# Kernel optimization log

Measured on AMD Instinct MI355X. Metric: run time of the kernel, lower is better.

The kernel has to match this reference:

```python
import jax, jax.numpy as jnp
import numpy as np


def _xcorr3x3_valid(x, k):
    # x: [B,H,W], k: [B,3,3] per-sample kernel; cross-correlation (matches F.conv2d), VALID padding
    B, H, W = x.shape
    out = jnp.zeros((B, H - 2, W - 2), dtype=x.dtype)
    for u in range(3):
        for v in range(3):
            out = out + x[:, u:u + H - 2, v:v + W - 2] * k[:, u, v, None, None]
    return out


def setup_inputs() -> dict:
    key = jax.random.key(0)
    ks = jax.random.split(key, 4)
    B, H, W = 256, 256, 256
    pred = jax.random.normal(ks[0], (B, H, W), dtype=jnp.float32)
    rhs = jax.random.normal(ks[1], (B, H - 2, W - 2), dtype=jnp.float32)
    Laplace_kernel = jax.random.normal(ks[2], (B, 3, 3), dtype=jnp.float32)
    Df_dr_kernel = jax.random.normal(ks[3], (B, 3, 3), dtype=jnp.float32)
    # physically sensible meshgrids: R in [1,2] (avoids div-by-zero), Z in [-1,1]
    r = jnp.linspace(1.0, 2.0, W, dtype=jnp.float32)
    z = jnp.linspace(-1.0, 1.0, H, dtype=jnp.float32)
    RR = jnp.broadcast_to(r[None, None, :], (B, H, W)).astype(jnp.float32)
    ZZ = jnp.broadcast_to(z[None, :, None], (B, H, W)).astype(jnp.float32)
    Gauss_kernel = (jnp.array([[1., 2., 1.], [2., 4., 2.], [1., 2., 1.]], dtype=jnp.float32) / 16.0)
    return {"pred": pred, "rhs": rhs, "Laplace_kernel": Laplace_kernel,
            "Df_dr_kernel": Df_dr_kernel, "RR": RR, "ZZ": ZZ, "Gauss_kernel": Gauss_kernel}


def reference(pred, rhs, Laplace_kernel, Df_dr_kernel, RR, ZZ, Gauss_kernel):
    # Lpsi, Dpsi_dr: per-sample 3x3 VALID stencils -> [B, H-2, W-2]
    Lpsi = _xcorr3x3_valid(pred, Laplace_kernel)
    Dpsi_dr = -_xcorr3x3_valid(pred, Df_dr_kernel)
    Dpsi_dr = Dpsi_dr / RR[:, 1:-1, 1:-1]
    lhs = Lpsi - Dpsi_dr
    hr = (RR[:, 1, 2] - RR[:, 1, 1])[:, None, None]
    hz = (ZZ[:, 2, 1] - ZZ[:, 1, 1])[:, None, None]
    alfa = -2.0 * (hr ** 2 + hz ** 2)
    GS_ope = lhs * alfa / (hr ** 2 * hz ** 2)
    # Gaussian smoothing, shared kernel, SAME padding (cross-correlation; kernel is symmetric)
    sm = jax.lax.conv_general_dilated(
        GS_ope[:, None, :, :], Gauss_kernel[None, None, :, :],
        window_strides=(1, 1), padding='SAME')
    GS_ope_smooth = -sm
    rhs_computed = -GS_ope_smooth[:, 0, :, :]
    return jnp.mean((rhs_computed - rhs) ** 2)
```

## Files before the change

kernel.cpp:

```cpp
#include <hip/hip_runtime.h>


__device__ __forceinline__ void g2lds16(const float* g, float* l) {
    __builtin_amdgcn_global_load_lds(
        (const __attribute__((address_space(1))) void*)g,
        (__attribute__((address_space(3))) void*)l,
        16 , 0, 0);
}

__global__ __launch_bounds__(256)
void pde_loss_kernel(const float* __restrict__ pred,
                     const float* __restrict__ rhs,
                     const float* __restrict__ KL,
                     const float* __restrict__ KD,
                     const float* __restrict__ RR,
                     const float* __restrict__ ZZ,
                     float* __restrict__ partials)
{
    constexpr int H = 256, W = 256, OH = 254, OW = 254;
    __shared__ float lds[36 * 256 + 16];
    __shared__ float wsum[4];

    const int tid = threadIdx.x;
    const int l   = tid & 63;
    const int wv  = tid >> 6;
    const int b   = blockIdx.x >> 3;
    const int rb  = (blockIdx.x & 7) * 32;
    const int o0  = rb + wv * 8;
    const int o1  = (o0 + 8 < OH) ? (o0 + 8) : OH;
    const int c0  = 4 * l;

    const size_t ib = (size_t)b * H * W;
    const float* predb = pred + ib;
    const float* rhsb  = rhs + (size_t)b * OH * OW;

    float2 r0[8], r1[8];
#pragma unroll
    for (int j = 0; j < 8; ++j) {
        r0[j] = make_float2(0.f, 0.f); r1[j] = make_float2(0.f, 0.f);
        if (o0 + j < o1) {
            const float* rr = rhsb + (size_t)(o0 + j) * OW + c0;
            r0[j] = *(const float2*)rr;
            if (c0 + 2 < OW) r1[j] = *(const float2*)(rr + 2);
        }
    }
    const float hr = RR[ib + W + 2] - RR[ib + W + 1];
    const float hz = ZZ[ib + 2 * W + 1] - ZZ[ib + W + 1];
    float klv[9], kdv[9];
#pragma unroll
    for (int t = 0; t < 9; ++t) { klv[t] = KL[b * 9 + t]; kdv[t] = KD[b * 9 + t]; }
    float4 invr;
    invr.x = RR[ib + W + (c0 + 1)];
    invr.y = RR[ib + W + (c0 + 2)];
    invr.z = RR[ib + W + (c0 + 3)];
    invr.w = RR[ib + W + ((c0 + 4 < W) ? (c0 + 4) : (W - 1))];

#pragma unroll
    for (int t = 0; t < 9; ++t) {
        const int j  = wv + 4 * t;
        const int gr = rb - 1 + j;
        if ((unsigned)gr < (unsigned)H)
            g2lds16(predb + (size_t)gr * W + c0, &lds[j * 256]);
    }

    const float hr2 = hr * hr, hz2 = hz * hz;
    const float s   = -2.0f * (hr2 + hz2) / (hr2 * hz2);
    invr.x = 1.0f / invr.x; invr.y = 1.0f / invr.y;
    invr.z = 1.0f / invr.z; invr.w = 1.0f / invr.w;
    const bool lastl = (l == 63);
    float4 c4[9];
#pragma unroll
    for (int t = 0; t < 9; ++t) {
        const float a = klv[t] * s, d = kdv[t] * s;
        c4[t].x = fmaf(d, invr.x, a);
        c4[t].y = fmaf(d, invr.y, a);
        c4[t].z = lastl ? 0.f : fmaf(d, invr.z, a);
        c4[t].w = lastl ? 0.f : fmaf(d, invr.w, a);
    }
    const float m23 = (c0 + 2 < OW) ? 1.f : 0.f;
    const float m0  = (l > 0) ? 1.f : 0.f;

    __syncthreads();

    const float* ldsw = &lds[wv * 8 * 256];
    float4 p0 = *(const float4*)&ldsw[0 * 256 + c0];
    float4 p1 = *(const float4*)&ldsw[1 * 256 + c0];
    float4 p2 = *(const float4*)&ldsw[2 * 256 + c0];
    float2 h0 = *(const float2*)&ldsw[0 * 256 + c0 + 4];
    float2 h1 = *(const float2*)&ldsw[1 * 256 + c0 + 4];
    float2 h2 = *(const float2*)&ldsw[2 * 256 + c0 + 4];

    float4 ghm2 = make_float4(0.f, 0.f, 0.f, 0.f);
    float4 ghm1 = make_float4(0.f, 0.f, 0.f, 0.f);
    float acc = 0.0f;

#define SROW(P, Hh, t0, t1, t2)                                               \
    gs.x = fmaf(P.x, c4[t0].x, fmaf(P.y, c4[t1].x, fmaf(P.z,  c4[t2].x, gs.x))); \
    gs.y = fmaf(P.y, c4[t0].y, fmaf(P.z, c4[t1].y, fmaf(P.w,  c4[t2].y, gs.y))); \
    gs.z = fmaf(P.z, c4[t0].z, fmaf(P.w, c4[t1].z, fmaf(Hh.x, c4[t2].z, gs.z))); \
    gs.w = fmaf(P.w, c4[t0].w, fmaf(Hh.x, c4[t1].w, fmaf(Hh.y, c4[t2].w, gs.w)));

#pragma unroll
    for (int K = 0; K < 10; ++K) {
        float4 pr = make_float4(0.f, 0.f, 0.f, 0.f);
        float2 hp = make_float2(0.f, 0.f);
        if (K < 9) {
            pr = *(const float4*)&ldsw[(K + 3) * 256 + c0];
            hp = *(const float2*)&ldsw[(K + 3) * 256 + c0 + 4];
        }

        const int g = o0 - 1 + K;
        float4 gs = make_float4(0.f, 0.f, 0.f, 0.f);
        if (g <= o1 && (unsigned)g < (unsigned)OH) {
            SROW(p0, h0, 0, 1, 2)
            SROW(p1, h1, 3, 4, 5)
            SROW(p2, h2, 6, 7, 8)
        }

        const float up = __shfl(gs.w, l - 1, 64) * m0;
        const float dn = __shfl(gs.x, l + 1, 64);
        float4 gh;
        gh.x = fmaf(2.f, gs.x, up   + gs.y);
        gh.y = fmaf(2.f, gs.y, gs.x + gs.z);
        gh.z = fmaf(2.f, gs.z, gs.y + gs.w);
        gh.w = fmaf(2.f, gs.w, gs.z + dn);

        if (K >= 2) {
            const int i = g - 1;
            if (i < o1) {
                const float smx = (ghm2.x + 2.f * ghm1.x + gh.x) * 0.0625f;
                const float smy = (ghm2.y + 2.f * ghm1.y + gh.y) * 0.0625f;
                const float smz = (ghm2.z + 2.f * ghm1.z + gh.z) * 0.0625f;
                const float smw = (ghm2.w + 2.f * ghm1.w + gh.w) * 0.0625f;
                const float dx = smx - r0[K - 2].x;
                const float dy = smy - r0[K - 2].y;
                const float dz = (smz - r1[K - 2].x) * m23;
                const float dw = (smw - r1[K - 2].y) * m23;
                acc = fmaf(dx, dx, acc);
                acc = fmaf(dy, dy, acc);
                acc = fmaf(dz, dz, acc);
                acc = fmaf(dw, dw, acc);
            }
        }

        p0 = p1; p1 = p2; p2 = pr;
        h0 = h1; h1 = h2; h2 = hp;
        ghm2 = ghm1; ghm1 = gh;
    }
#undef SROW

#pragma unroll
    for (int off = 32; off > 0; off >>= 1)
        acc += __shfl_down(acc, off, 64);
    if (l == 0) wsum[wv] = acc;
    __syncthreads();
    if (tid == 0)
        partials[blockIdx.x] = (wsum[0] + wsum[1]) + (wsum[2] + wsum[3]);
}

__global__ __launch_bounds__(256)
void reduce_kernel(const float* __restrict__ partials, float* __restrict__ out,
                   int n, float inv_n)
{
    const int tid = threadIdx.x;
    float a = 0.0f;
    for (int i = tid; i < n; i += 256) a += partials[i];
#pragma unroll
    for (int off = 32; off > 0; off >>= 1)
        a += __shfl_down(a, off, 64);
    __shared__ float w[4];
    if ((tid & 63) == 0) w[tid >> 6] = a;
    __syncthreads();
    if (tid == 0) out[0] = ((w[0] + w[1]) + (w[2] + w[3])) * inv_n;
}

extern "C" void kernel_launch(void* const* d_in, const int* in_sizes, int n_in,
                              void* d_out, int out_size, void* d_ws, size_t ws_size,
                              hipStream_t stream) {
    const float* pred = (const float*)d_in[0];
    const float* rhs  = (const float*)d_in[1];
    const float* KL   = (const float*)d_in[2];
    const float* KD   = (const float*)d_in[3];
    const float* RR   = (const float*)d_in[4];
    const float* ZZ   = (const float*)d_in[5];
    float* out = (float*)d_out;

    const int B = in_sizes[2] / 9;
    const int nblocks = B * 8;
    const float inv_n = 1.0f / ((float)B * 254.0f * 254.0f);

    float* partials = (float*)d_ws;
    pde_loss_kernel<<<dim3(nblocks), dim3(256), 0, stream>>>(
        pred, rhs, KL, KD, RR, ZZ, partials);
    reduce_kernel<<<dim3(1), dim3(256), 0, stream>>>(partials, out, nblocks, inv_n);
}
```

Measured before the change: 213.5 us.

## Stream pred and rhs rows through per-wave LDS ring buffers with async loads

Each wave now processes a 16-row strip, using 4 waves per block and half as many blocks. Pred and rhs rows are streamed into per-wave ring buffers in LDS with global_load_lds, and explicit vmcnt waits replace the block-wide barrier and the upfront rhs register preload. The aim is to overlap global loads with the stencil compute, cut halo re-reads, and lower register pressure. The risks are fewer blocks, which reduces parallelism, and fragile hand-counted vmcnt values. The last rhs row is special-cased because the clamped staging cannot read it as a float4.

```diff
diff --git a/kernel.cpp b/kernel.cpp
--- a/kernel.cpp
+++ b/kernel.cpp
@@ -18,60 +18,43 @@
                      float* __restrict__ partials)
 {
     constexpr int H = 256, W = 256, OH = 254, OW = 254;
-    __shared__ float lds[36 * 256 + 16];
+    constexpr int PR = 5, PSTR = 260;
+    constexpr int RS = 4, RSTR = 256;
+    constexpr int WREG = PR * PSTR + RS * RSTR;
+    __shared__ float lds[4 * WREG];
     __shared__ float wsum[4];
 
     const int tid = threadIdx.x;
     const int l   = tid & 63;
     const int wv  = tid >> 6;
-    const int b   = blockIdx.x >> 3;
-    const int rb  = (blockIdx.x & 7) * 32;
-    const int o0  = rb + wv * 8;
-    const int o1  = (o0 + 8 < OH) ? (o0 + 8) : OH;
-    const int c0  = 4 * l;
+    const int b   = blockIdx.x >> 2;
+    const int strip = (blockIdx.x & 3) * 4 + wv;
+    const int o0 = strip * 16;
+    const int o1 = (o0 + 16 < OH) ? (o0 + 16) : OH;
+    const int c0 = 4 * l;
 
     const size_t ib = (size_t)b * H * W;
     const float* predb = pred + ib;
     const float* rhsb  = rhs + (size_t)b * OH * OW;
-
-    float2 r0[8], r1[8];
-#pragma unroll
-    for (int j = 0; j < 8; ++j) {
-        r0[j] = make_float2(0.f, 0.f); r1[j] = make_float2(0.f, 0.f);
-        if (o0 + j < o1) {
-            const float* rr = rhsb + (size_t)(o0 + j) * OW + c0;
-            r0[j] = *(const float2*)rr;
-            if (c0 + 2 < OW) r1[j] = *(const float2*)(rr + 2);
-        }
-    }
-    const float hr = RR[ib + W + 2] - RR[ib + W + 1];
-    const float hz = ZZ[ib + 2 * W + 1] - ZZ[ib + W + 1];
-    float klv[9], kdv[9];
-#pragma unroll
-    for (int t = 0; t < 9; ++t) { klv[t] = KL[b * 9 + t]; kdv[t] = KD[b * 9 + t]; }
-    float4 invr;
-    invr.x = RR[ib + W + (c0 + 1)];
-    invr.y = RR[ib + W + (c0 + 2)];
-    invr.z = RR[ib + W + (c0 + 3)];
-    invr.w = RR[ib + W + ((c0 + 4 < W) ? (c0 + 4) : (W - 1))];
-
-#pragma unroll
-    for (int t = 0; t < 9; ++t) {
-        const int j  = wv + 4 * t;
-        const int gr = rb - 1 + j;
-        if ((unsigned)gr < (unsigned)H)
-            g2lds16(predb + (size_t)gr * W + c0, &lds[j * 256]);
-    }
-
+    float* wls = &lds[wv * WREG];
+
+    if (l < PR)
+        *(float4*)(wls + l * PSTR + 256) = make_float4(0.f, 0.f, 0.f, 0.f);
+
+    const float hr  = RR[ib + W + 2] - RR[ib + W + 1];
+    const float hz  = ZZ[ib + 2 * W + 1] - ZZ[ib + W + 1];
     const float hr2 = hr * hr, hz2 = hz * hz;
     const float s   = -2.0f * (hr2 + hz2) / (hr2 * hz2);
-    invr.x = 1.0f / invr.x; invr.y = 1.0f / invr.y;
-    invr.z = 1.0f / invr.z; invr.w = 1.0f / invr.w;
+    float4 invr;
+    invr.x = 1.0f / RR[ib + W + (c0 + 1)];
+    invr.y = 1.0f / RR[ib + W + (c0 + 2)];
+    invr.z = 1.0f / RR[ib + W + (c0 + 3)];
+    invr.w = 1.0f / RR[ib + W + ((c0 + 4 < W) ? (c0 + 4) : (W - 1))];
     const bool lastl = (l == 63);
     float4 c4[9];
 #pragma unroll
     for (int t = 0; t < 9; ++t) {
-        const float a = klv[t] * s, d = kdv[t] * s;
+        const float a = KL[b * 9 + t] * s, d = KD[b * 9 + t] * s;
         c4[t].x = fmaf(d, invr.x, a);
         c4[t].y = fmaf(d, invr.y, a);
         c4[t].z = lastl ? 0.f : fmaf(d, invr.z, a);
@@ -80,19 +63,33 @@
     const float m23 = (c0 + 2 < OW) ? 1.f : 0.f;
     const float m0  = (l > 0) ? 1.f : 0.f;
 
-    __syncthreads();
-
-    const float* ldsw = &lds[wv * 8 * 256];
-    float4 p0 = *(const float4*)&ldsw[0 * 256 + c0];
-    float4 p1 = *(const float4*)&ldsw[1 * 256 + c0];
-    float4 p2 = *(const float4*)&ldsw[2 * 256 + c0];
-    float2 h0 = *(const float2*)&ldsw[0 * 256 + c0 + 4];
-    float2 h1 = *(const float2*)&ldsw[1 * 256 + c0 + 4];
-    float2 h2 = *(const float2*)&ldsw[2 * 256 + c0 + 4];
-
-    float4 ghm2 = make_float4(0.f, 0.f, 0.f, 0.f);
-    float4 ghm1 = make_float4(0.f, 0.f, 0.f, 0.f);
-    float acc = 0.0f;
+    float2 rl0 = make_float2(0.f, 0.f), rl1 = make_float2(0.f, 0.f);
+    if (o1 == OH) {
+        const float* rr = rhsb + (size_t)(OH - 1) * OW + c0;
+        rl0 = *(const float2*)rr;
+        if (c0 + 2 < OW) rl1 = *(const float2*)(rr + 2);
+    }
+
+    auto stage_pred = [&](int j) {
+        int gr = o0 - 1 + j;
+        gr = (gr < 0) ? 0 : ((gr > H - 1) ? H - 1 : gr);
+        g2lds16(predb + (size_t)gr * W + c0, wls + (j % PR) * PSTR);
+    };
+    auto stage_rhs = [&](int j) {
+        int gr = o0 + j;
+        gr = (gr > OH - 2) ? (OH - 2) : gr;
+        g2lds16(rhsb + (size_t)gr * OW + c0, wls + PR * PSTR + (j % RS) * RSTR);
+    };
+
+    __builtin_amdgcn_sched_barrier(0);
+    asm volatile("s_waitcnt vmcnt(0)" ::: "memory");
+    stage_pred(0); __builtin_amdgcn_sched_barrier(0);
+    stage_pred(1); __builtin_amdgcn_sched_barrier(0);
+    stage_pred(2); __builtin_amdgcn_sched_barrier(0);
+    stage_pred(3); __builtin_amdgcn_sched_barrier(0);
+    stage_pred(4); __builtin_amdgcn_sched_barrier(0);
+    stage_rhs(0);  __builtin_amdgcn_sched_barrier(0);
+    stage_rhs(1);  __builtin_amdgcn_sched_barrier(0);
 
 #define SROW(P, Hh, t0, t1, t2)                                               \
     gs.x = fmaf(P.x, c4[t0].x, fmaf(P.y, c4[t1].x, fmaf(P.z,  c4[t2].x, gs.x))); \
@@ -100,18 +97,34 @@
     gs.z = fmaf(P.z, c4[t0].z, fmaf(P.w, c4[t1].z, fmaf(Hh.x, c4[t2].z, gs.z))); \
     gs.w = fmaf(P.w, c4[t0].w, fmaf(Hh.x, c4[t1].w, fmaf(Hh.y, c4[t2].w, gs.w)));
 
-#pragma unroll
-    for (int K = 0; K < 10; ++K) {
-        float4 pr = make_float4(0.f, 0.f, 0.f, 0.f);
-        float2 hp = make_float2(0.f, 0.f);
-        if (K < 9) {
-            pr = *(const float4*)&ldsw[(K + 3) * 256 + c0];
-            hp = *(const float2*)&ldsw[(K + 3) * 256 + c0 + 4];
+    float4 p0, p1, p2;
+    float2 h0, h1, h2;
+    float4 ghm2 = make_float4(0.f, 0.f, 0.f, 0.f);
+    float4 ghm1 = make_float4(0.f, 0.f, 0.f, 0.f);
+    float acc = 0.0f;
+
+#pragma unroll
+    for (int K = 0; K < 18; ++K) {
+        if (K == 0 || K == 15)  asm volatile("s_waitcnt vmcnt(4)" ::: "memory");
+        else if (K <= 14)       asm volatile("s_waitcnt vmcnt(5)" ::: "memory");
+        else if (K == 16)       asm volatile("s_waitcnt vmcnt(2)" ::: "memory");
+        else                    asm volatile("s_waitcnt vmcnt(0)" ::: "memory");
+
+        if (K == 0) {
+            p0 = *(const float4*)(wls + 0 * PSTR + c0);
+            h0 = *(const float2*)(wls + 0 * PSTR + c0 + 4);
+            p1 = *(const float4*)(wls + 1 * PSTR + c0);
+            h1 = *(const float2*)(wls + 1 * PSTR + c0 + 4);
+        }
+        {
+            const int sl = (K + 2) % PR;
+            p2 = *(const float4*)(wls + sl * PSTR + c0);
+            h2 = *(const float2*)(wls + sl * PSTR + c0 + 4);
         }
 
         const int g = o0 - 1 + K;
         float4 gs = make_float4(0.f, 0.f, 0.f, 0.f);
-        if (g <= o1 && (unsigned)g < (unsigned)OH) {
+        if ((unsigned)g < (unsigned)OH) {
             SROW(p0, h0, 0, 1, 2)
             SROW(p1, h1, 3, 4, 5)
             SROW(p2, h2, 6, 7, 8)
@@ -126,16 +139,20 @@
         gh.w = fmaf(2.f, gs.w, gs.z + dn);
 
         if (K >= 2) {
-            const int i = g - 1;
+            const int i = o0 + K - 2;
             if (i < o1) {
+                const float* rr = wls + PR * PSTR + ((K - 2) % RS) * RSTR + c0;
+                float4 rv = *(const float4*)rr;
+                if (i == OH - 1)
+                    rv = make_float4(rl0.x, rl0.y, rl1.x, rl1.y);
                 const float smx = (ghm2.x + 2.f * ghm1.x + gh.x) * 0.0625f;
                 const float smy = (ghm2.y + 2.f * ghm1.y + gh.y) * 0.0625f;
                 const float smz = (ghm2.z + 2.f * ghm1.z + gh.z) * 0.0625f;
                 const float smw = (ghm2.w + 2.f * ghm1.w + gh.w) * 0.0625f;
-                const float dx = smx - r0[K - 2].x;
-                const float dy = smy - r0[K - 2].y;
-                const float dz = (smz - r1[K - 2].x) * m23;
-                const float dw = (smw - r1[K - 2].y) * m23;
+                const float dx = smx - rv.x;
+                const float dy = smy - rv.y;
+                const float dz = (smz - rv.z) * m23;
+                const float dw = (smw - rv.w) * m23;
                 acc = fmaf(dx, dx, acc);
                 acc = fmaf(dy, dy, acc);
                 acc = fmaf(dz, dz, acc);
@@ -143,9 +160,13 @@
             }
         }
 
-        p0 = p1; p1 = p2; p2 = pr;
-        h0 = h1; h1 = h2; h2 = hp;
+        p0 = p1; p1 = p2; h0 = h1; h1 = h2;
         ghm2 = ghm1; ghm1 = gh;
+
+        if (K <= 14) stage_pred(K + 5);
+        __builtin_amdgcn_sched_barrier(0);
+        if (K <= 13) stage_rhs(K + 2);
+        __builtin_amdgcn_sched_barrier(0);
     }
 #undef SROW
 
@@ -186,7 +207,7 @@
     float* out = (float*)d_out;
 
     const int B = in_sizes[2] / 9;
-    const int nblocks = B * 8;
+    const int nblocks = B * 4;
     const float inv_n = 1.0f / ((float)B * 254.0f * 254.0f);
 
     float* partials = (float*)d_ws;
```

Result: no change. 217.2 us (+1.7%).
